# Kernel tuning notes

Measured on AMD Instinct MI355X. Metric: run time of the kernel, lower is better.

The kernel has to match this reference:

```python
import jax, jax.numpy as jnp
import numpy as np

OUT_FEATURES = 4096
IN_FEATURES = 4096
GROUP_SIZE = 128
NUM_GROUPS = IN_FEATURES // GROUP_SIZE  # 32
PACKED_SIZE = OUT_FEATURES * IN_FEATURES // 8  # 2097152


def setup_inputs() -> dict:
    key = jax.random.key(0)
    k1, k2, k3, k4 = jax.random.split(key, 4)
    x = jax.random.normal(k1, (2, 512, IN_FEATURES), dtype=jnp.float32)
    # random packed 4-bit weights (8 nibbles per int32)
    w_packed = jax.random.randint(k2, (PACKED_SIZE,), jnp.iinfo(jnp.int32).min,
                                  jnp.iinfo(jnp.int32).max, dtype=jnp.int32)
    w_scale = jax.random.uniform(k3, (OUT_FEATURES, NUM_GROUPS), dtype=jnp.float32) * 0.05
    w_zero = jax.random.randint(k4, (OUT_FEATURES, NUM_GROUPS), 0, 8, dtype=jnp.int32)
    return {"x": x, "w_packed": w_packed, "w_scale": w_scale, "w_zero": w_zero}


def _unpack_dequant(w_packed, w_scale, w_zero):
    # Extract 8 nibbles per int32: (v >> (i*4)) & 0xF, i = 0..7
    shifts = jnp.arange(8, dtype=jnp.int32) * 4
    nibbles = (w_packed[:, None] >> shifts[None, :]) & 15  # [packed, 8]
    w4 = nibbles.reshape(-1)  # [out*in], values 0..15
    w4 = jnp.where(w4 >= 8, w4 - 16, w4)  # signed 4-bit -> [-8, 7]
    w_int = w4.reshape(OUT_FEATURES, NUM_GROUPS, GROUP_SIZE).astype(jnp.float32)
    # per-(row, group) dequant: (q - zero) * scale
    w = (w_int - w_zero[:, :, None].astype(jnp.float32)) * w_scale[:, :, None]
    return w.reshape(OUT_FEATURES, IN_FEATURES)


def reference(x, w_packed, w_scale, w_zero):
    weight = _unpack_dequant(w_packed, w_scale, w_zero).astype(x.dtype)
    # F.linear: y = x @ W^T
    return jnp.einsum('bsi,oi->bso', x, weight)
```

## Files before the change

kernel.cpp:

```cpp
#include <hip/hip_runtime.h>
#include <hip/hip_bf16.h>
#include <stdint.h>

#define IN_F 4096
#define OUT_F 4096
#define NG 32

typedef __attribute__((ext_vector_type(8))) short short8;
typedef __attribute__((ext_vector_type(4))) float floatx4;

__global__ __launch_bounds__(256) void dequant_kernel(
    const int* __restrict__ wp, const float* __restrict__ scale,
    const int* __restrict__ zero, __hip_bfloat16* __restrict__ Wb) {
  int p = blockIdx.x * 256 + threadIdx.x;
  int row = p >> 9;
  int g = (p >> 4) & 31;
  float s = scale[row * NG + g];
  float zs = (float)zero[row * NG + g] * s;
  unsigned v = (unsigned)wp[p];
  union { __hip_bfloat16 h[8]; uint4 u4; } o;
#pragma unroll
  for (int i = 0; i < 8; ++i) {
    int q = (int)((v >> (4 * i)) & 15u);
    q -= (q >= 8) ? 16 : 0;
    o.h[i] = __float2bfloat16((float)q * s - zs);
  }
  *(uint4*)(Wb + (size_t)p * 8) = o.u4;
}

__global__ __launch_bounds__(256) void convert_kernel(
    const float* __restrict__ x, __hip_bfloat16* __restrict__ xb) {
  int i = blockIdx.x * 256 + threadIdx.x;
  float4 v = ((const float4*)x)[i];
  union { __hip_bfloat16 h[4]; uint2 u; } o;
  o.h[0] = __float2bfloat16(v.x);
  o.h[1] = __float2bfloat16(v.y);
  o.h[2] = __float2bfloat16(v.z);
  o.h[3] = __float2bfloat16(v.w);
  ((uint2*)xb)[i] = o.u;
}

#define BM 128
#define BN 128
#define BK 64
#define SPLITK 2

__global__ __launch_bounds__(256) void gemm_bt(
    const __hip_bfloat16* __restrict__ A, const __hip_bfloat16* __restrict__ Bt,
    float* __restrict__ C0, float* __restrict__ C1, int M, int N, int K) {
  __shared__ short Alds[BM * BK];
  __shared__ short Blds[BN * BK];

  int t = threadIdx.x;
  int wave = t >> 6, lane = t & 63;
  int wm = (wave >> 1) * 64, wn = (wave & 1) * 64;
  int r = lane & 15, quad = lane >> 4;
  int bm = blockIdx.y * BM, bn = blockIdx.x * BN;
  int kz = blockIdx.z * (K / SPLITK);
  int kend = kz + K / SPLITK;

  floatx4 acc[4][4] = {};

  const __hip_bfloat16* Ag = A + (size_t)bm * K;
  const __hip_bfloat16* Bg = Bt + (size_t)bn * K;

  for (int k0 = kz; k0 < kend; k0 += BK) {
    __syncthreads();
#pragma unroll
    for (int j = 0; j < 4; ++j) {
      int c = t + 256 * j;
      int row = c >> 3, kc = c & 7;
      const __hip_bfloat16* ga = Ag + (size_t)row * K + k0 + kc * 8;
      const __hip_bfloat16* gb = Bg + (size_t)row * K + k0 + kc * 8;
      __builtin_amdgcn_global_load_lds(
          (const __attribute__((address_space(1))) void*)ga,
          (__attribute__((address_space(3))) void*)(&Alds[c * 8]), 16, 0, 0);
      __builtin_amdgcn_global_load_lds(
          (const __attribute__((address_space(1))) void*)gb,
          (__attribute__((address_space(3))) void*)(&Blds[c * 8]), 16, 0, 0);
    }
    __syncthreads();

#pragma unroll
    for (int ks = 0; ks < 2; ++ks) {
      int kk = ks * 32;
      short8 af[4], bf[4];
#pragma unroll
      for (int mi = 0; mi < 4; ++mi)
        af[mi] = *(const short8*)&Alds[(wm + mi * 16 + r) * BK + kk + quad * 8];
#pragma unroll
      for (int ni = 0; ni < 4; ++ni)
        bf[ni] = *(const short8*)&Blds[(wn + ni * 16 + r) * BK + kk + quad * 8];
#pragma unroll
      for (int mi = 0; mi < 4; ++mi)
#pragma unroll
        for (int ni = 0; ni < 4; ++ni)
          acc[mi][ni] = __builtin_amdgcn_mfma_f32_16x16x32_bf16(
              af[mi], bf[ni], acc[mi][ni], 0, 0, 0);
    }
  }

  float* C = (blockIdx.z == 0) ? C0 : C1;
#pragma unroll
  for (int mi = 0; mi < 4; ++mi) {
#pragma unroll
    for (int ni = 0; ni < 4; ++ni) {
#pragma unroll
      for (int i = 0; i < 4; ++i) {
        int grow = bm + wm + mi * 16 + quad * 4 + i;
        int gcol = bn + wn + ni * 16 + r;
        C[(size_t)grow * N + gcol] = acc[mi][ni][i];
      }
    }
  }
}

__global__ __launch_bounds__(256) void reduce_kernel(
    float* __restrict__ out, const float* __restrict__ part) {
  int i = blockIdx.x * 256 + threadIdx.x;
  float4 a = ((const float4*)out)[i];
  float4 b = ((const float4*)part)[i];
  a.x += b.x; a.y += b.y; a.z += b.z; a.w += b.w;
  ((float4*)out)[i] = a;
}

extern "C" void kernel_launch(void* const* d_in, const int* in_sizes, int n_in,
                              void* d_out, int out_size, void* d_ws, size_t ws_size,
                              hipStream_t stream) {
  const float* x = (const float*)d_in[0];
  const int* wp = (const int*)d_in[1];
  const float* wscale = (const float*)d_in[2];
  const int* wzero = (const int*)d_in[3];
  float* out = (float*)d_out;

  int M = in_sizes[0] / IN_F;

  __hip_bfloat16* Wb = (__hip_bfloat16*)d_ws;
  __hip_bfloat16* Xb = (__hip_bfloat16*)((char*)d_ws + (size_t)OUT_F * IN_F * 2);
  float* Cpart = (float*)((char*)d_ws + (size_t)OUT_F * IN_F * 2 + (size_t)M * IN_F * 2);

  dequant_kernel<<<(OUT_F * IN_F / 8) / 256, 256, 0, stream>>>(wp, wscale, wzero, Wb);
  convert_kernel<<<(M * IN_F / 4) / 256, 256, 0, stream>>>(x, Xb);

  dim3 grid(OUT_F / BN, M / BM, SPLITK);
  gemm_bt<<<grid, 256, 0, stream>>>(Xb, Wb, out, Cpart, M, OUT_F, IN_F);

  reduce_kernel<<<(M * OUT_F / 4) / 256, 256, 0, stream>>>(out, Cpart);
}
```

Before: 138.8 us.

## Fuse 4-bit weight dequantization into GEMM B-tile loading

```diff
diff --git a/kernel.cpp b/kernel.cpp
--- a/kernel.cpp
+++ b/kernel.cpp
@@ -9,47 +9,31 @@
 typedef __attribute__((ext_vector_type(8))) short short8;
 typedef __attribute__((ext_vector_type(4))) float floatx4;
 
-__global__ __launch_bounds__(256) void dequant_kernel(
-    const int* __restrict__ wp, const float* __restrict__ scale,
-    const int* __restrict__ zero, __hip_bfloat16* __restrict__ Wb) {
-  int p = blockIdx.x * 256 + threadIdx.x;
-  int row = p >> 9;
-  int g = (p >> 4) & 31;
-  float s = scale[row * NG + g];
-  float zs = (float)zero[row * NG + g] * s;
-  unsigned v = (unsigned)wp[p];
-  union { __hip_bfloat16 h[8]; uint4 u4; } o;
-#pragma unroll
-  for (int i = 0; i < 8; ++i) {
-    int q = (int)((v >> (4 * i)) & 15u);
-    q -= (q >= 8) ? 16 : 0;
-    o.h[i] = __float2bfloat16((float)q * s - zs);
-  }
-  *(uint4*)(Wb + (size_t)p * 8) = o.u4;
-}
-
 __global__ __launch_bounds__(256) void convert_kernel(
     const float* __restrict__ x, __hip_bfloat16* __restrict__ xb) {
   int i = blockIdx.x * 256 + threadIdx.x;
-  float4 v = ((const float4*)x)[i];
-  union { __hip_bfloat16 h[4]; uint2 u; } o;
-  o.h[0] = __float2bfloat16(v.x);
-  o.h[1] = __float2bfloat16(v.y);
-  o.h[2] = __float2bfloat16(v.z);
-  o.h[3] = __float2bfloat16(v.w);
-  ((uint2*)xb)[i] = o.u;
+  float4 v0 = ((const float4*)x)[i * 2];
+  float4 v1 = ((const float4*)x)[i * 2 + 1];
+  union { __hip_bfloat16 h[8]; uint4 u4; } o;
+  o.h[0] = __float2bfloat16(v0.x); o.h[1] = __float2bfloat16(v0.y);
+  o.h[2] = __float2bfloat16(v0.z); o.h[3] = __float2bfloat16(v0.w);
+  o.h[4] = __float2bfloat16(v1.x); o.h[5] = __float2bfloat16(v1.y);
+  o.h[6] = __float2bfloat16(v1.z); o.h[7] = __float2bfloat16(v1.w);
+  ((uint4*)xb)[i] = o.u4;
 }
 
 #define BM 128
 #define BN 128
 #define BK 64
 #define SPLITK 2
+#define BSTRIDE 68
 
 __global__ __launch_bounds__(256) void gemm_bt(
-    const __hip_bfloat16* __restrict__ A, const __hip_bfloat16* __restrict__ Bt,
+    const __hip_bfloat16* __restrict__ A, const uint32_t* __restrict__ wp,
+    const float* __restrict__ scale, const int* __restrict__ zero,
     float* __restrict__ C0, float* __restrict__ C1, int M, int N, int K) {
   __shared__ short Alds[BM * BK];
-  __shared__ short Blds[BN * BK];
+  __shared__ short Blds[BN * BSTRIDE];
 
   int t = threadIdx.x;
   int wave = t >> 6, lane = t & 63;
@@ -59,25 +43,47 @@
   int kz = blockIdx.z * (K / SPLITK);
   int kend = kz + K / SPLITK;
 
+  int row2 = t >> 1, half = t & 1;
+  int wrow = bn + row2;
+  const uint4* wrow4 = (const uint4*)(wp + (size_t)wrow * (IN_F / 8));
+
   floatx4 acc[4][4] = {};
 
   const __hip_bfloat16* Ag = A + (size_t)bm * K;
-  const __hip_bfloat16* Bg = Bt + (size_t)bn * K;
+
+  uint4 bp = wrow4[(kz >> 5) + half];
+  float s = scale[wrow * NG + (kz >> 7)];
+  float zs = (float)zero[wrow * NG + (kz >> 7)] * s;
 
   for (int k0 = kz; k0 < kend; k0 += BK) {
     __syncthreads();
 #pragma unroll
     for (int j = 0; j < 4; ++j) {
       int c = t + 256 * j;
-      int row = c >> 3, kc = c & 7;
-      const __hip_bfloat16* ga = Ag + (size_t)row * K + k0 + kc * 8;
-      const __hip_bfloat16* gb = Bg + (size_t)row * K + k0 + kc * 8;
+      int rowA = c >> 3, kc = c & 7;
       __builtin_amdgcn_global_load_lds(
-          (const __attribute__((address_space(1))) void*)ga,
+          (const __attribute__((address_space(1))) void*)(Ag + (size_t)rowA * K + k0 + kc * 8),
           (__attribute__((address_space(3))) void*)(&Alds[c * 8]), 16, 0, 0);
-      __builtin_amdgcn_global_load_lds(
-          (const __attribute__((address_space(1))) void*)gb,
-          (__attribute__((address_space(3))) void*)(&Blds[c * 8]), 16, 0, 0);
+    }
+    int kb = half * 32;
+#pragma unroll
+    for (int e = 0; e < 4; ++e) {
+      uint32_t w = (&bp.x)[e];
+      union { __hip_bfloat16 h[8]; uint4 u4; } o;
+#pragma unroll
+      for (int i = 0; i < 8; ++i) {
+        int q = ((int)(w << (28 - 4 * i))) >> 28;
+        o.h[i] = __float2bfloat16((float)q * s - zs);
+      }
+      *(uint4*)&Blds[row2 * BSTRIDE + kb + e * 8] = o.u4;
+    }
+    int kn = k0 + BK;
+    if (kn < kend) {
+      bp = wrow4[(kn >> 5) + half];
+      if ((kn & 127) == 0) {
+        s = scale[wrow * NG + (kn >> 7)];
+        zs = (float)zero[wrow * NG + (kn >> 7)] * s;
+      }
     }
     __syncthreads();
 
@@ -90,7 +96,7 @@
         af[mi] = *(const short8*)&Alds[(wm + mi * 16 + r) * BK + kk + quad * 8];
 #pragma unroll
       for (int ni = 0; ni < 4; ++ni)
-        bf[ni] = *(const short8*)&Blds[(wn + ni * 16 + r) * BK + kk + quad * 8];
+        bf[ni] = *(const short8*)&Blds[(wn + ni * 16 + r) * BSTRIDE + kk + quad * 8];
 #pragma unroll
       for (int mi = 0; mi < 4; ++mi)
 #pragma unroll
@@ -100,7 +106,7 @@
     }
   }
 
-  float* C = (blockIdx.z == 0) ? C0 : C1;
+  float* Cz = (blockIdx.z == 0) ? C0 : C1;
 #pragma unroll
   for (int mi = 0; mi < 4; ++mi) {
 #pragma unroll
@@ -109,7 +115,7 @@
       for (int i = 0; i < 4; ++i) {
         int grow = bm + wm + mi * 16 + quad * 4 + i;
         int gcol = bn + wn + ni * 16 + r;
-        C[(size_t)grow * N + gcol] = acc[mi][ni][i];
+        Cz[(size_t)grow * N + gcol] = acc[mi][ni][i];
       }
     }
   }
@@ -128,22 +134,20 @@
                               void* d_out, int out_size, void* d_ws, size_t ws_size,
                               hipStream_t stream) {
   const float* x = (const float*)d_in[0];
-  const int* wp = (const int*)d_in[1];
+  const uint32_t* wp = (const uint32_t*)d_in[1];
   const float* wscale = (const float*)d_in[2];
   const int* wzero = (const int*)d_in[3];
   float* out = (float*)d_out;
 
   int M = in_sizes[0] / IN_F;
 
-  __hip_bfloat16* Wb = (__hip_bfloat16*)d_ws;
-  __hip_bfloat16* Xb = (__hip_bfloat16*)((char*)d_ws + (size_t)OUT_F * IN_F * 2);
-  float* Cpart = (float*)((char*)d_ws + (size_t)OUT_F * IN_F * 2 + (size_t)M * IN_F * 2);
+  __hip_bfloat16* Xb = (__hip_bfloat16*)d_ws;
+  float* Cpart = (float*)((char*)d_ws + (size_t)M * IN_F * 2);
 
-  dequant_kernel<<<(OUT_F * IN_F / 8) / 256, 256, 0, stream>>>(wp, wscale, wzero, Wb);
-  convert_kernel<<<(M * IN_F / 4) / 256, 256, 0, stream>>>(x, Xb);
+  convert_kernel<<<(M * IN_F / 8) / 256, 256, 0, stream>>>(x, Xb);
 
   dim3 grid(OUT_F / BN, M / BM, SPLITK);
-  gemm_bt<<<grid, 256, 0, stream>>>(Xb, Wb, out, Cpart, M, OUT_F, IN_F);
+  gemm_bt<<<grid, 256, 0, stream>>>(Xb, wp, wscale, wzero, out, Cpart, M, OUT_F, IN_F);
 
   reduce_kernel<<<(M * OUT_F / 4) / 256, 256, 0, stream>>>(out, Cpart);
 }
```

Result: slower. 147.7 us (+6.4%).
